# Optimization experiments

Hardware: AMD Instinct MI355X
Metric: run time of the kernel (lower is better)

## Reference

```python
import jax, jax.numpy as jnp
import numpy as np

N_NODES = 500_000
FEAT_DIM = 256
NUM_CLASSES = 128
NUM_SEGMENTS = 2048


def setup_inputs() -> dict:
    key = jax.random.key(0)
    k_h, k_b, k_w1, k_b1, k_w2, k_b2 = jax.random.split(key, 6)
    H = jax.random.normal(k_h, (N_NODES, FEAT_DIM), dtype=jnp.float32)
    batch = jnp.sort(jax.random.randint(k_b, (N_NODES,), 0, NUM_SEGMENTS, dtype=jnp.int64))
    # MLP(feat_dim, feat_dim, num_classes): Linear -> ReLU -> Linear
    s1 = 1.0 / np.sqrt(FEAT_DIM)
    W1 = jax.random.uniform(k_w1, (FEAT_DIM, FEAT_DIM), jnp.float32, -s1, s1)
    b1 = jax.random.uniform(k_b1, (FEAT_DIM,), jnp.float32, -s1, s1)
    W2 = jax.random.uniform(k_w2, (FEAT_DIM, NUM_CLASSES), jnp.float32, -s1, s1)
    b2 = jax.random.uniform(k_b2, (NUM_CLASSES,), jnp.float32, -s1, s1)
    return {"H": H, "batch": batch, "num_segments": NUM_SEGMENTS,
            "W1": W1, "b1": b1, "W2": W2, "b2": b2}


def segment_softmax(x, seg_ids, num_segments):
    # numerically stable softmax over rows sharing the same segment id (dim 0)
    seg_max = jax.ops.segment_max(x, seg_ids, num_segments=num_segments)  # [S, C]
    shifted = x - seg_max[seg_ids]
    ex = jnp.exp(shifted)
    seg_sum = jax.ops.segment_sum(ex, seg_ids, num_segments=num_segments)  # [S, C]
    return ex / seg_sum[seg_ids]


def reference(H, batch, num_segments, W1, b1, W2, b2):
    # MLP projection: feat_dim -> feat_dim -> num_classes
    h = jax.nn.relu(jnp.einsum('nd,df->nf', H, W1) + b1)
    logits = jnp.einsum('nf,fc->nc', h, W2) + b2  # [N, num_classes]
    # discrete=True path: segment-wise softmax keyed by `batch`
    probs = segment_softmax(logits, batch, num_segments)
    return (logits, probs)
```

## Files before the change

kernel.cpp:

```cpp
#include <hip/hip_runtime.h>
#include <hip/hip_bf16.h>

#define N_NODES 500000
#define FEAT 256
#define NCLS 128
#define NSEG 2048

typedef __attribute__((ext_vector_type(8))) short bfrag8;
typedef __attribute__((ext_vector_type(4))) float facc4;

__device__ __forceinline__ unsigned short f2bf(float f) {
    unsigned int u = __float_as_uint(f);
    u += 0x7FFFu + ((u >> 16) & 1u);
    return (unsigned short)(u >> 16);
}

__global__ void prep_kernel(const float* __restrict__ W1, const float* __restrict__ W2,
                            short* __restrict__ W1t, short* __restrict__ W2t) {
    int idx = blockIdx.x * 256 + threadIdx.x;
    if (idx < FEAT * FEAT) {
        int d = idx >> 8, f = idx & 255;
        W1t[f * FEAT + d] = (short)f2bf(W1[idx]);
    }
    if (idx < FEAT * NCLS) {
        int d = idx >> 7, c = idx & 127;
        W2t[c * FEAT + d] = (short)f2bf(W2[idx]);
    }
}

__global__ __launch_bounds__(256, 2)
void mlp_kernel(const float* __restrict__ H, const short* __restrict__ W1t,
                const float* __restrict__ b1, const short* __restrict__ W2t,
                const float* __restrict__ b2, float* __restrict__ logits) {
    __shared__ short tile[128 * 256];

    const int tid  = threadIdx.x;
    const int lane = tid & 63;
    const int l15  = lane & 15;
    const int quad = lane >> 4;
    const int wave = tid >> 6;
    const int row0 = blockIdx.x * 128;

    #pragma unroll
    for (int it = 0; it < 32; ++it) {
        int flat = it * 1024 + tid * 4;
        int r = flat >> 8, c = flat & 255;
        float4 v = {0.f, 0.f, 0.f, 0.f};
        if (row0 + r < N_NODES)
            v = *reinterpret_cast<const float4*>(H + (size_t)(row0 + r) * FEAT + c);
        short4 s;
        s.x = (short)f2bf(v.x); s.y = (short)f2bf(v.y);
        s.z = (short)f2bf(v.z); s.w = (short)f2bf(v.w);
        int g = (c >> 3) ^ (r & 7);
        *reinterpret_cast<short4*>(&tile[r * 256 + g * 8 + (c & 7)]) = s;
    }
    __syncthreads();

    const int r0 = wave * 32 + l15;
    const int r1 = wave * 32 + 16 + l15;
    const int rx = l15 & 7;

    facc4 acc[2][16];
    #pragma unroll
    for (int rt = 0; rt < 2; ++rt)
        #pragma unroll
        for (int ct = 0; ct < 16; ++ct)
            acc[rt][ct] = (facc4){0.f, 0.f, 0.f, 0.f};

    #pragma unroll
    for (int kk = 0; kk < 8; ++kk) {
        int kb = kk * 32 + quad * 8;
        int gs = ((kb >> 3) ^ rx) << 3;
        bfrag8 a0 = *reinterpret_cast<const bfrag8*>(&tile[r0 * 256 + gs]);
        bfrag8 a1 = *reinterpret_cast<const bfrag8*>(&tile[r1 * 256 + gs]);
        #pragma unroll
        for (int ct = 0; ct < 16; ++ct) {
            bfrag8 b = *reinterpret_cast<const bfrag8*>(&W1t[(ct * 16 + l15) * FEAT + kb]);
            acc[0][ct] = __builtin_amdgcn_mfma_f32_16x16x32_bf16(a0, b, acc[0][ct], 0, 0, 0);
            acc[1][ct] = __builtin_amdgcn_mfma_f32_16x16x32_bf16(a1, b, acc[1][ct], 0, 0, 0);
        }
    }

    #pragma unroll
    for (int ct = 0; ct < 16; ++ct) {
        float bias = b1[ct * 16 + l15];
        int c = ct * 16 + l15;
        #pragma unroll
        for (int rt = 0; rt < 2; ++rt) {
            int rbase = wave * 32 + rt * 16 + quad * 4;
            #pragma unroll
            for (int i = 0; i < 4; ++i) {
                float v = fmaxf(acc[rt][ct][i] + bias, 0.f);
                int r = rbase + i;
                int g = (c >> 3) ^ (r & 7);
                tile[r * 256 + g * 8 + (c & 7)] = (short)f2bf(v);
            }
        }
    }

    facc4 acc2[2][8];
    #pragma unroll
    for (int rt = 0; rt < 2; ++rt)
        #pragma unroll
        for (int ct = 0; ct < 8; ++ct)
            acc2[rt][ct] = (facc4){0.f, 0.f, 0.f, 0.f};

    #pragma unroll
    for (int kk = 0; kk < 8; ++kk) {
        int kb = kk * 32 + quad * 8;
        int gs = ((kb >> 3) ^ rx) << 3;
        bfrag8 a0 = *reinterpret_cast<const bfrag8*>(&tile[r0 * 256 + gs]);
        bfrag8 a1 = *reinterpret_cast<const bfrag8*>(&tile[r1 * 256 + gs]);
        #pragma unroll
        for (int ct = 0; ct < 8; ++ct) {
            bfrag8 b = *reinterpret_cast<const bfrag8*>(&W2t[(ct * 16 + l15) * FEAT + kb]);
            acc2[0][ct] = __builtin_amdgcn_mfma_f32_16x16x32_bf16(a0, b, acc2[0][ct], 0, 0, 0);
            acc2[1][ct] = __builtin_amdgcn_mfma_f32_16x16x32_bf16(a1, b, acc2[1][ct], 0, 0, 0);
        }
    }

    #pragma unroll
    for (int ct = 0; ct < 8; ++ct) {
        float bias = b2[ct * 16 + l15];
        int c = ct * 16 + l15;
        #pragma unroll
        for (int rt = 0; rt < 2; ++rt) {
            int rbase = row0 + wave * 32 + rt * 16 + quad * 4;
            #pragma unroll
            for (int i = 0; i < 4; ++i) {
                int r = rbase + i;
                if (r < N_NODES)
                    logits[(size_t)r * NCLS + c] = acc2[rt][ct][i] + bias;
            }
        }
    }
}

__global__ void seg_sum_kernel(const float* __restrict__ logits,
                               const int* __restrict__ batch,
                               float* __restrict__ Lsum) {
    int seg = blockIdx.x;
    int lo = 0, hi = N_NODES;
    while (lo < hi) { int m = (lo + hi) >> 1; if (batch[m] < seg) lo = m + 1; else hi = m; }
    int start = lo;
    hi = N_NODES;
    while (lo < hi) { int m = (lo + hi) >> 1; if (batch[m] < seg + 1) lo = m + 1; else hi = m; }
    int end = lo;

    int t = threadIdx.x;
    int c = t & 127, half = t >> 7;
    float s = 0.f;
    for (int r = start + half; r < end; r += 2)
        s += __expf(logits[(size_t)r * NCLS + c]);

    __shared__ float red[256];
    red[t] = s;
    __syncthreads();
    if (half == 0) Lsum[seg * NCLS + c] = red[c] + red[c + 128];
}

__global__ void probs_kernel(const float* __restrict__ logits,
                             const int* __restrict__ batch,
                             const float* __restrict__ Lsum,
                             float* __restrict__ probs) {
    int idx = blockIdx.x * 256 + threadIdx.x;
    int n = idx >> 5;
    if (n >= N_NODES) return;
    int c4 = (idx & 31) << 2;
    int seg = batch[n];
    float4 lg = *reinterpret_cast<const float4*>(&logits[(size_t)n * NCLS + c4]);
    float4 L  = *reinterpret_cast<const float4*>(&Lsum[(size_t)seg * NCLS + c4]);
    float4 p;
    p.x = __expf(lg.x) / L.x; p.y = __expf(lg.y) / L.y;
    p.z = __expf(lg.z) / L.z; p.w = __expf(lg.w) / L.w;
    *reinterpret_cast<float4*>(&probs[(size_t)n * NCLS + c4]) = p;
}

extern "C" void kernel_launch(void* const* d_in, const int* in_sizes, int n_in,
                              void* d_out, int out_size, void* d_ws, size_t ws_size,
                              hipStream_t stream) {
    const float* H     = (const float*)d_in[0];
    const int*   batch = (const int*)d_in[1];
    const float* W1    = (const float*)d_in[3];
    const float* b1    = (const float*)d_in[4];
    const float* W2    = (const float*)d_in[5];
    const float* b2    = (const float*)d_in[6];

    float* out    = (float*)d_out;
    float* logits = out;
    float* probs  = out + (size_t)N_NODES * NCLS;

    char* ws = (char*)d_ws;
    short* W1t  = (short*)ws;
    short* W2t  = (short*)(ws + 131072);
    float* Lsum = (float*)(ws + 131072 + 65536);

    prep_kernel<<<256, 256, 0, stream>>>(W1, W2, W1t, W2t);
    mlp_kernel<<<(N_NODES + 127) / 128, 256, 0, stream>>>(H, W1t, b1, W2t, b2, logits);
    seg_sum_kernel<<<NSEG, 256, 0, stream>>>(logits, batch, Lsum);
    probs_kernel<<<(N_NODES * 32 + 255) / 256, 256, 0, stream>>>(logits, batch, Lsum, probs);
}
```

Before: 1.419 ms.

## Load H fragments directly from global and vectorize segment-sum reduction

The MLP kernel no longer stages the whole 128x256 H tile in shared memory behind a block-wide barrier. Each wave now reads its A fragments straight from global memory as float4 pairs, converts them to bf16 in registers, and uses a private per-wave LDS buffer only for the hidden activations. This removes the staging pass and the __syncthreads, but the per-lane global reads are strided by row and less coalesced. Separately, seg_sum_kernel now reads float4s with 8 row-strided groups and reduces through shared memory, giving more memory parallelism per segment.

```diff
diff --git a/kernel.cpp b/kernel.cpp
--- a/kernel.cpp
+++ b/kernel.cpp
@@ -32,33 +32,20 @@
 void mlp_kernel(const float* __restrict__ H, const short* __restrict__ W1t,
                 const float* __restrict__ b1, const short* __restrict__ W2t,
                 const float* __restrict__ b2, float* __restrict__ logits) {
-    __shared__ short tile[128 * 256];
+    __shared__ short hb[4][32 * 256];
 
     const int tid  = threadIdx.x;
     const int lane = tid & 63;
     const int l15  = lane & 15;
     const int quad = lane >> 4;
     const int wave = tid >> 6;
-    const int row0 = blockIdx.x * 128;
-
-    #pragma unroll
-    for (int it = 0; it < 32; ++it) {
-        int flat = it * 1024 + tid * 4;
-        int r = flat >> 8, c = flat & 255;
-        float4 v = {0.f, 0.f, 0.f, 0.f};
-        if (row0 + r < N_NODES)
-            v = *reinterpret_cast<const float4*>(H + (size_t)(row0 + r) * FEAT + c);
-        short4 s;
-        s.x = (short)f2bf(v.x); s.y = (short)f2bf(v.y);
-        s.z = (short)f2bf(v.z); s.w = (short)f2bf(v.w);
-        int g = (c >> 3) ^ (r & 7);
-        *reinterpret_cast<short4*>(&tile[r * 256 + g * 8 + (c & 7)]) = s;
-    }
-    __syncthreads();
-
-    const int r0 = wave * 32 + l15;
-    const int r1 = wave * 32 + 16 + l15;
-    const int rx = l15 & 7;
+    const int row0 = blockIdx.x * 128 + wave * 32;
+    short* hw = hb[wave];
+
+    const int rg0 = min(row0 + l15,      N_NODES - 1);
+    const int rg1 = min(row0 + 16 + l15, N_NODES - 1);
+    const float* rA0 = H + (size_t)rg0 * FEAT;
+    const float* rA1 = H + (size_t)rg1 * FEAT;
 
     facc4 acc[2][16];
     #pragma unroll
@@ -69,10 +56,16 @@
 
     #pragma unroll
     for (int kk = 0; kk < 8; ++kk) {
-        int kb = kk * 32 + quad * 8;
-        int gs = ((kb >> 3) ^ rx) << 3;
-        bfrag8 a0 = *reinterpret_cast<const bfrag8*>(&tile[r0 * 256 + gs]);
-        bfrag8 a1 = *reinterpret_cast<const bfrag8*>(&tile[r1 * 256 + gs]);
+        const int kb = kk * 32 + quad * 8;
+        float4 lo0 = *reinterpret_cast<const float4*>(rA0 + kb);
+        float4 hi0 = *reinterpret_cast<const float4*>(rA0 + kb + 4);
+        float4 lo1 = *reinterpret_cast<const float4*>(rA1 + kb);
+        float4 hi1 = *reinterpret_cast<const float4*>(rA1 + kb + 4);
+        bfrag8 a0, a1;
+        a0[0]=(short)f2bf(lo0.x); a0[1]=(short)f2bf(lo0.y); a0[2]=(short)f2bf(lo0.z); a0[3]=(short)f2bf(lo0.w);
+        a0[4]=(short)f2bf(hi0.x); a0[5]=(short)f2bf(hi0.y); a0[6]=(short)f2bf(hi0.z); a0[7]=(short)f2bf(hi0.w);
+        a1[0]=(short)f2bf(lo1.x); a1[1]=(short)f2bf(lo1.y); a1[2]=(short)f2bf(lo1.z); a1[3]=(short)f2bf(lo1.w);
+        a1[4]=(short)f2bf(hi1.x); a1[5]=(short)f2bf(hi1.y); a1[6]=(short)f2bf(hi1.z); a1[7]=(short)f2bf(hi1.w);
         #pragma unroll
         for (int ct = 0; ct < 16; ++ct) {
             bfrag8 b = *reinterpret_cast<const bfrag8*>(&W1t[(ct * 16 + l15) * FEAT + kb]);
@@ -87,17 +80,18 @@
         int c = ct * 16 + l15;
         #pragma unroll
         for (int rt = 0; rt < 2; ++rt) {
-            int rbase = wave * 32 + rt * 16 + quad * 4;
+            int rbase = rt * 16 + quad * 4;
             #pragma unroll
             for (int i = 0; i < 4; ++i) {
                 float v = fmaxf(acc[rt][ct][i] + bias, 0.f);
                 int r = rbase + i;
                 int g = (c >> 3) ^ (r & 7);
-                tile[r * 256 + g * 8 + (c & 7)] = (short)f2bf(v);
+                hw[r * 256 + g * 8 + (c & 7)] = (short)f2bf(v);
             }
         }
     }
 
+    const int rx = l15 & 7;
     facc4 acc2[2][8];
     #pragma unroll
     for (int rt = 0; rt < 2; ++rt)
@@ -107,10 +101,10 @@
 
     #pragma unroll
     for (int kk = 0; kk < 8; ++kk) {
-        int kb = kk * 32 + quad * 8;
-        int gs = ((kb >> 3) ^ rx) << 3;
-        bfrag8 a0 = *reinterpret_cast<const bfrag8*>(&tile[r0 * 256 + gs]);
-        bfrag8 a1 = *reinterpret_cast<const bfrag8*>(&tile[r1 * 256 + gs]);
+        const int kb = kk * 32 + quad * 8;
+        const int gs = ((kb >> 3) ^ rx) << 3;
+        bfrag8 a0 = *reinterpret_cast<const bfrag8*>(&hw[l15 * 256 + gs]);
+        bfrag8 a1 = *reinterpret_cast<const bfrag8*>(&hw[(16 + l15) * 256 + gs]);
         #pragma unroll
         for (int ct = 0; ct < 8; ++ct) {
             bfrag8 b = *reinterpret_cast<const bfrag8*>(&W2t[(ct * 16 + l15) * FEAT + kb]);
@@ -125,7 +119,7 @@
         int c = ct * 16 + l15;
         #pragma unroll
         for (int rt = 0; rt < 2; ++rt) {
-            int rbase = row0 + wave * 32 + rt * 16 + quad * 4;
+            int rbase = row0 + rt * 16 + quad * 4;
             #pragma unroll
             for (int i = 0; i < 4; ++i) {
                 int r = rbase + i;
@@ -148,15 +142,27 @@
     int end = lo;
 
     int t = threadIdx.x;
-    int c = t & 127, half = t >> 7;
-    float s = 0.f;
-    for (int r = start + half; r < end; r += 2)
-        s += __expf(logits[(size_t)r * NCLS + c]);
-
-    __shared__ float red[256];
-    red[t] = s;
+    int cg = t & 31;
+    int rs = t >> 5;
+    float4 s = {0.f, 0.f, 0.f, 0.f};
+    for (int r = start + rs; r < end; r += 8) {
+        float4 v = *reinterpret_cast<const float4*>(&logits[(size_t)r * NCLS + cg * 4]);
+        s.x += __expf(v.x); s.y += __expf(v.y);
+        s.z += __expf(v.z); s.w += __expf(v.w);
+    }
+
+    __shared__ float4 red[8][32];
+    red[rs][cg] = s;
     __syncthreads();
-    if (half == 0) Lsum[seg * NCLS + c] = red[c] + red[c + 128];
+    if (t < 32) {
+        float4 a = red[0][t];
+        #pragma unroll
+        for (int k = 1; k < 8; ++k) {
+            float4 b = red[k][t];
+            a.x += b.x; a.y += b.y; a.z += b.z; a.w += b.w;
+        }
+        *reinterpret_cast<float4*>(&Lsum[(size_t)seg * NCLS + t * 4]) = a;
+    }
 }
 
 __global__ void probs_kernel(const float* __restrict__ logits,
```

Result: faster. 1.308 ms (-7.8%).
